# Kernel optimization log

Measured on AMD Instinct MI355X. Metric: run time of the kernel, lower is better.

Reference implementation:

```python
import jax, jax.numpy as jnp
import numpy as np

D = 768   # embedding_dimensions (richness) — hardcoded in source
H = 3     # heads — hardcoded in source


def setup_inputs() -> dict:
    key = jax.random.key(0)
    ks = jax.random.split(key, 12)
    s = 1.0 / np.sqrt(D)
    s3 = 1.0 / np.sqrt(H * D)
    return {
        "x": jax.random.normal(ks[0], (4, 2048, D), dtype=jnp.float32),
        # QKV projections: Linear(D, D*H), stored as (in, out)
        "Wq": jax.random.uniform(ks[1], (D, D * H), jnp.float32, -s, s),
        "bq": jax.random.uniform(ks[2], (D * H,), jnp.float32, -s, s),
        "Wk": jax.random.uniform(ks[3], (D, D * H), jnp.float32, -s, s),
        "bk": jax.random.uniform(ks[4], (D * H,), jnp.float32, -s, s),
        "Wv": jax.random.uniform(ks[5], (D, D * H), jnp.float32, -s, s),
        "bv": jax.random.uniform(ks[6], (D * H,), jnp.float32, -s, s),
        # final projection: Linear(H*D, D)
        "Wo": jax.random.uniform(ks[7], (H * D, D), jnp.float32, -s3, s3),
        "bo": jax.random.uniform(ks[8], (D,), jnp.float32, -s3, s3),
        # FFN: Linear(D, D) + LeakyReLU
        "Wf": jax.random.uniform(ks[9], (D, D), jnp.float32, -s, s),
        "bf": jax.random.uniform(ks[10], (D,), jnp.float32, -s, s),
    }


def reference(x, Wq, bq, Wk, bk, Wv, bv, Wo, bo, Wf, bf):
    B, S, _ = x.shape
    # QKV: [B,S,H*D] -> [B,H,S,D]  (head dim == full D, as in source)
    q = (x @ Wq + bq).reshape(B, S, H, D).transpose(0, 2, 1, 3)
    k = (x @ Wk + bk).reshape(B, S, H, D).transpose(0, 2, 1, 3)
    v = (x @ Wv + bv).reshape(B, S, H, D).transpose(0, 2, 1, 3)
    # unscaled attention scores (source applies no 1/sqrt(d))
    scores = jnp.einsum('bhqd,bhkd->bhqk', q, k)
    # faithful masking: tril of the scores themselves, fill zeros with -99999
    masked = jnp.where(jnp.tril(scores) == 0, jnp.float32(-99999.0), scores)
    attn = jax.nn.softmax(masked, axis=-1)
    o = jnp.einsum('bhqk,bhkd->bhqd', attn, v)
    o = o.transpose(0, 2, 1, 3).reshape(B, S, H * D)
    a = o @ Wo + bo
    # "normalisation": subtract global mean over the whole tensor
    n = a - jnp.mean(a)
    y = n + x  # residual
    return jax.nn.leaky_relu(y @ Wf + bf, negative_slope=0.01)
```

## Files before the change

kernel.cpp:

```cpp
#include <hip/hip_runtime.h>
#include <hip/hip_bf16.h>

typedef __attribute__((ext_vector_type(8))) __bf16 bf16x8;
typedef __attribute__((ext_vector_type(4))) float f32x4;
typedef unsigned short u16;

#define DEV static __device__ __forceinline__

#define BAR() asm volatile("s_barrier" ::: "memory")
#define LGKM0() asm volatile("s_waitcnt lgkmcnt(0)" ::: "memory")
#define VMCNT6() asm volatile("s_waitcnt vmcnt(6)" ::: "memory")
#define VMCNT3() asm volatile("s_waitcnt vmcnt(3)" ::: "memory")
#define VMCNT0() asm volatile("s_waitcnt vmcnt(0)" ::: "memory")

DEV void load_lds16(const void* g, void* l) {
  __builtin_amdgcn_global_load_lds(
      (const __attribute__((address_space(1))) unsigned int*)g,
      (__attribute__((address_space(3))) unsigned int*)l, 16, 0, 0);
}

DEV u16 bf16bits(float v) {
  __hip_bfloat16 h = __float2bfloat16(v);
  return __builtin_bit_cast(u16, h);
}

DEV float bf2f(u16 u) {
  return __builtin_bit_cast(float, (unsigned)u << 16);
}

DEV bf16x8 rdfrag(const u16* region, int row, int ks, int l) {
  const int cb = (((ks << 6) | ((l >> 4) << 4)) ^ ((l & 7) << 4));
  return *(const bf16x8*)((const char*)region + row * 128 + cb);
}

struct OffN { unsigned long long a[12], b[12], c[12]; };

enum { G128_SC = 0, G128_PV = 1, G128_PLAIN = 2, G128_LEAKY = 3 };

__global__ __launch_bounds__(512, 1) void k_qkv256(
    const u16* __restrict__ A, const u16* __restrict__ B,
    const float* __restrict__ bias, u16* __restrict__ C, u16* __restrict__ Vt)
{
  int flat = blockIdx.y * 27 + blockIdx.x;
  flat = (flat & 7) * 108 + (flat >> 3);
  const int n0 = (flat % 27) * 256, m0 = (flat / 27) * 256;
  const int lda = 768, ldb = 768, nkt = 12;

  __shared__ u16 smem[65536];
  u16* As0 = smem;
  u16* Bs0 = smem + 32768;

  const int tid = threadIdx.x;
  const int l = tid & 63;
  const int wid = tid >> 6;
  const int wm = wid >> 1, wn = wid & 1;

  const int r0s = wid * 16 + (l >> 3);
  const int ces = ((l & 7) ^ (l >> 3)) << 3;
  const size_t aR0 = (size_t)(m0 + r0s) * lda + ces;
  const size_t aR1 = aR0 + (size_t)8 * lda;
  const size_t bR0 = (size_t)(n0 + r0s) * ldb + ces;
  const size_t bR1 = bR0 + (size_t)8 * ldb;
  const size_t hA = (size_t)128 * lda, hB = (size_t)128 * ldb;
  const int dst0 = wid * 1024 + l * 8, dst1 = dst0 + 512;

#define STAGE_A(bf, h, kkv) do {                                 \
    u16* Lp = As0 + (bf) * 16384 + (h) * 8192;                   \
    load_lds16(A + aR0 + ((h) ? hA : 0) + (kkv), Lp + dst0);     \
    load_lds16(A + aR1 + ((h) ? hA : 0) + (kkv), Lp + dst1);     \
  } while (0)
#define STAGE_B(bf, h, kkv) do {                                 \
    u16* Lp = Bs0 + (bf) * 16384 + (h) * 8192;                   \
    load_lds16(B + bR0 + ((h) ? hB : 0) + (kkv), Lp + dst0);     \
    load_lds16(B + bR1 + ((h) ? hB : 0) + (kkv), Lp + dst1);     \
  } while (0)

  f32x4 acc[2][2][2][4] = {};
  bf16x8 af[2][2], bA[4][2], bB[4][2];

#define MFMA16(QM, QN, BARR)                                                  \
    __builtin_amdgcn_s_setprio(1);                                            \
    _Pragma("unroll") for (int ks = 0; ks < 2; ks++)                          \
      _Pragma("unroll") for (int fm = 0; fm < 2; fm++)                        \
        _Pragma("unroll") for (int fn = 0; fn < 4; fn++)                      \
          acc[QM][QN][fm][fn] = __builtin_amdgcn_mfma_f32_16x16x32_bf16(      \
              af[fm][ks], BARR[fn][ks], acc[QM][QN][fm][fn], 0, 0, 0);        \
    __builtin_amdgcn_s_setprio(0);

#define RD_A(half)                                                            \
    _Pragma("unroll") for (int fm = 0; fm < 2; fm++)                          \
      _Pragma("unroll") for (int ks = 0; ks < 2; ks++)                        \
        af[fm][ks] = rdfrag(half, wm * 32 + fm * 16 + (l & 15), ks, l);
#define RD_B(dstv, half)                                                      \
    _Pragma("unroll") for (int fn = 0; fn < 4; fn++)                          \
      _Pragma("unroll") for (int ks = 0; ks < 2; ks++)                        \
        dstv[fn][ks] = rdfrag(half, wn * 64 + fn * 16 + (l & 15), ks, l);

  STAGE_A(0, 0, 0); STAGE_B(0, 0, 0); STAGE_B(0, 1, 0); STAGE_A(0, 1, 0);
  STAGE_A(1, 0, 64); STAGE_B(1, 0, 64); STAGE_B(1, 1, 64);
  VMCNT3();
  BAR();

  for (int t = 0; t < nkt; ++t) {
    const int cur = t & 1, nxt = cur ^ 1;
    const int kk1 = (t + 1) << 6, kk2 = (t + 2) << 6;
    const bool s1 = (t + 1 < nkt), s2 = (t + 2 < nkt);
    RD_A(As0 + cur * 16384);
    RD_B(bA, Bs0 + cur * 16384);
    if (s1) STAGE_A(nxt, 1, kk1);
    BAR(); LGKM0();
    MFMA16(0, 0, bA);
    BAR();
    RD_B(bB, Bs0 + cur * 16384 + 8192);
    if (s2) STAGE_A(cur, 0, kk2);
    BAR(); LGKM0();
    MFMA16(0, 1, bB);
    BAR();
    RD_A(As0 + cur * 16384 + 8192);
    if (s2) STAGE_B(cur, 0, kk2);
    BAR(); LGKM0();
    MFMA16(1, 1, bB);
    BAR();
    if (s2) STAGE_B(cur, 1, kk2);
    BAR();
    MFMA16(1, 0, bA);
    if (s2) { VMCNT3(); } else { VMCNT0(); }
    BAR();
  }
#undef RD_A
#undef RD_B
#undef MFMA16
#undef STAGE_A
#undef STAGE_B

  __syncthreads();
  const int sel = n0 >= 4608 ? 2 : (n0 >= 2304 ? 1 : 0);
  const int r0c = (l >> 4) << 2;
  if (sel == 2) {
#pragma unroll
    for (int Qm = 0; Qm < 2; Qm++)
#pragma unroll
      for (int Qn = 0; Qn < 2; Qn++)
#pragma unroll
        for (int fn = 0; fn < 4; fn++) {
          const int coll = Qn * 128 + wn * 64 + fn * 16 + (l & 15);
          const float bv = bias[n0 + coll];
#pragma unroll
          for (int fm = 0; fm < 2; fm++)
#pragma unroll
            for (int r = 0; r < 4; r++) {
              const int rowl = Qm * 128 + wm * 32 + fm * 16 + r0c + r;
              smem[coll * 256 + (rowl ^ (((coll >> 2) & 3) << 4))] =
                  bf16bits(acc[Qm][Qn][fm][fn][r] + bv);
            }
        }
    __syncthreads();
    const int n0v = n0 - 4608;
    const int h = n0v / 768, d0l = n0v % 768;
    const int b = m0 >> 11, sbase = m0 & 2047;
    u16* Cb = Vt + ((size_t)(b * 3 + h) * 768 + d0l) * 2048 + sbase;
#pragma unroll
    for (int j = 0; j < 16; j++) {
      const int dr = j * 16 + (tid >> 5);
      const int c = (tid & 31) * 8;
      bf16x8 v = *(const bf16x8*)&smem[dr * 256 + (c ^ (((dr >> 2) & 3) << 4))];
      *(bf16x8*)&Cb[(size_t)dr * 2048 + c] = v;
    }
  } else {
#pragma unroll
    for (int Qm = 0; Qm < 2; Qm++)
#pragma unroll
      for (int Qn = 0; Qn < 2; Qn++)
#pragma unroll
        for (int fn = 0; fn < 4; fn++) {
          const int coll = Qn * 128 + wn * 64 + fn * 16 + (l & 15);
          const float bv = bias[n0 + coll];
#pragma unroll
          for (int fm = 0; fm < 2; fm++)
#pragma unroll
            for (int r = 0; r < 4; r++) {
              const int rowl = Qm * 128 + wm * 32 + fm * 16 + r0c + r;
              smem[rowl * 256 + (coll ^ (((rowl >> 2) & 3) << 4))] =
                  bf16bits(acc[Qm][Qn][fm][fn][r] + bv);
            }
        }
    __syncthreads();
    u16* Cb = C + (size_t)sel * (8192ull * 2304) + (n0 - sel * 2304);
#pragma unroll
    for (int j = 0; j < 16; j++) {
      const int rowl = j * 16 + (tid >> 5);
      const int c = (tid & 31) * 8;
      bf16x8 v = *(const bf16x8*)&smem[rowl * 256 + (c ^ (((rowl >> 2) & 3) << 4))];
      *(bf16x8*)&Cb[(size_t)(m0 + rowl) * 2304 + c] = v;
    }
  }
}

template<int MODE>
__global__ __launch_bounds__(512, 1) void k_g128(
    const u16* __restrict__ Abase, const u16* __restrict__ Bbase,
    const float* __restrict__ bias, void* __restrict__ Cbase,
    float* __restrict__ part,
    long lda, long ldb, long ldc, int K, OffN off)
{
  int m0, n0, z, r = 0, rb = 0, nkt, arow0, brow0;
  const u16 *A, *B;
  if (MODE == G128_SC) {
    r = blockIdx.y; z = blockIdx.z;
    rb = r >> 1;
    if ((int)blockIdx.x > rb) return;
    m0 = r * 128; n0 = blockIdx.x * 256;
    nkt = K >> 6;
    A = Abase + off.a[z]; B = Bbase + off.b[z];
    arow0 = m0; brow0 = n0;
  } else if (MODE == G128_PV) {
    r = 15 - (int)blockIdx.y;
    rb = r >> 1;
    z = blockIdx.x / 3;
    m0 = r * 128; n0 = (blockIdx.x % 3) * 256;
    nkt = (rb + 1) * 4;
    lda = (long)(rb + 1) * 256;
    A = Abase + off.a[z] + (size_t)32768 * rb * (rb + 1);
    B = Bbase + off.b[z];
    arow0 = (r & 1) * 128; brow0 = n0;
  } else {
    z = 0;
    m0 = blockIdx.y * 128; n0 = blockIdx.x * 256;
    nkt = K >> 6;
    A = Abase; B = Bbase;
    arow0 = m0; brow0 = n0;
  }

  __shared__ u16 smem[73728];

  const int tid = threadIdx.x;
  const int l = tid & 63;
  const int wid = tid >> 6;
  const int wm = wid & 1;
  const int wn = wid >> 1;

  const int ces = ((tid & 7) ^ ((tid >> 3) & 7)) << 3;
  const u16* aS = A + (size_t)(arow0 + (tid >> 3)) * lda + ces;
  const u16* bS = B + (size_t)(brow0 + (tid >> 3)) * ldb + ces;
  const int t8 = tid * 8;

#define STG(buf, kkv) do {                                       \
    u16* Lp = smem + (buf) * 24576;                              \
    load_lds16(aS + (kkv),             Lp + t8);                 \
    load_lds16(aS + 64 * lda + (kkv),  Lp + 4096 + t8);          \
    load_lds16(bS + (kkv),             Lp + 8192 + t8);          \
    load_lds16(bS + 64 * ldb + (kkv),  Lp + 12288 + t8);         \
    load_lds16(bS + 128 * ldb + (kkv), Lp + 16384 + t8);         \
    load_lds16(bS + 192 * ldb + (kkv), Lp + 20480 + t8);         \
  } while (0)

  f32x4 acc[4][4] = {};
  bf16x8 af[4][2], bf[4][2];

  STG(0, 0);
  STG(1, 64);
  VMCNT6();
  BAR();

  for (int t = 0; t < nkt; ++t) {
    const u16* Ar = smem + (t % 3) * 24576;
    const u16* Br = Ar + 8192;
#pragma unroll
    for (int fm = 0; fm < 4; fm++)
#pragma unroll
      for (int ks = 0; ks < 2; ks++)
        af[fm][ks] = rdfrag(Ar, wm * 64 + fm * 16 + (l & 15), ks, l);
#pragma unroll
    for (int fn = 0; fn < 4; fn++)
#pragma unroll
      for (int ks = 0; ks < 2; ks++)
        bf[fn][ks] = rdfrag(Br, wn * 64 + fn * 16 + (l & 15), ks, l);
    const bool s2 = (t + 2 < nkt);
    if (s2) STG((t + 2) % 3, (t + 2) << 6);
    BAR(); LGKM0();
    __builtin_amdgcn_s_setprio(1);
#pragma unroll
    for (int ks = 0; ks < 2; ks++)
#pragma unroll
      for (int fm = 0; fm < 4; fm++)
#pragma unroll
        for (int fn = 0; fn < 4; fn++)
          acc[fm][fn] = __builtin_amdgcn_mfma_f32_16x16x32_bf16(
              af[fm][ks], bf[fn][ks], acc[fm][fn], 0, 0, 0);
    __builtin_amdgcn_s_setprio(0);
    if (s2) { VMCNT6(); } else if (t + 1 < nkt) { VMCNT0(); }
    BAR();
  }
#undef STG

  const int r0c = (l >> 4) << 2;
  if (MODE == G128_SC) {
    float mx4[4][4], s4[4][4];
#pragma unroll
    for (int fm = 0; fm < 4; fm++)
#pragma unroll
      for (int rr = 0; rr < 4; rr++) {
        const int gi = m0 + wm * 64 + fm * 16 + r0c + rr;
        float mv = -1e30f;
#pragma unroll
        for (int fn = 0; fn < 4; fn++) {
          const int gc = n0 + wn * 64 + fn * 16 + (l & 15);
          float v = (gc <= gi) ? acc[fm][fn][rr] : -1e30f;
          acc[fm][fn][rr] = v;
          mv = fmaxf(mv, v);
        }
        mx4[fm][rr] = mv;
      }
#pragma unroll
    for (int o = 1; o < 16; o <<= 1)
#pragma unroll
      for (int fm = 0; fm < 4; fm++)
#pragma unroll
        for (int rr = 0; rr < 4; rr++)
          mx4[fm][rr] = fmaxf(mx4[fm][rr], __shfl_xor(mx4[fm][rr], o, 64));
    float* redm = (float*)smem;
    float* reds = redm + 512;
#pragma unroll
    for (int fm = 0; fm < 4; fm++)
#pragma unroll
      for (int rr = 0; rr < 4; rr++)
        if ((l & 15) == fm * 4 + rr)
          redm[(wm * 64 + fm * 16 + r0c + rr) * 4 + wn] = mx4[fm][rr];
    __syncthreads();
#pragma unroll
    for (int fm = 0; fm < 4; fm++)
#pragma unroll
      for (int rr = 0; rr < 4; rr++) {
        const int rowl = wm * 64 + fm * 16 + r0c + rr;
        f32x4 rm = *(const f32x4*)&redm[rowl * 4];
        const float tm = fmaxf(fmaxf(rm[0], rm[1]), fmaxf(rm[2], rm[3]));
        mx4[fm][rr] = tm;
        float ss = 0.f;
#pragma unroll
        for (int fn = 0; fn < 4; fn++) {
          const float e = expf(acc[fm][fn][rr] - tm);
          acc[fm][fn][rr] = e;
          ss += e;
        }
        s4[fm][rr] = ss;
      }
#pragma unroll
    for (int o = 1; o < 16; o <<= 1)
#pragma unroll
      for (int fm = 0; fm < 4; fm++)
#pragma unroll
        for (int rr = 0; rr < 4; rr++)
          s4[fm][rr] += __shfl_xor(s4[fm][rr], o, 64);
#pragma unroll
    for (int fm = 0; fm < 4; fm++)
#pragma unroll
      for (int rr = 0; rr < 4; rr++)
        if ((l & 15) == fm * 4 + rr)
          reds[(wm * 64 + fm * 16 + r0c + rr) * 4 + wn] = s4[fm][rr];
    __syncthreads();
    if (wn == 0) {
#pragma unroll
      for (int fm = 0; fm < 4; fm++)
#pragma unroll
        for (int rr = 0; rr < 4; rr++)
          if ((l & 15) == fm * 4 + rr) {
            const int rowl = wm * 64 + fm * 16 + r0c + rr;
            f32x4 rs = *(const f32x4*)&reds[rowl * 4];
            float2 pw;
            pw.x = mx4[fm][rr];
            pw.y = rs[0] + rs[1] + rs[2] + rs[3];
            *(float2*)&part[(size_t)z * 32768 +
                            ((size_t)(m0 + rowl) * 8 + blockIdx.x) * 2] = pw;
          }
    }
    __syncthreads();
#pragma unroll
    for (int fn = 0; fn < 4; fn++) {
      const int coll = wn * 64 + fn * 16 + (l & 15);
#pragma unroll
      for (int fm = 0; fm < 4; fm++)
#pragma unroll
        for (int rr = 0; rr < 4; rr++) {
          const int rowl = wm * 64 + fm * 16 + r0c + rr;
          smem[rowl * 256 + (coll ^ (((rowl >> 2) & 3) << 4))] =
              bf16bits(acc[fm][fn][rr]);
        }
    }
    __syncthreads();
    u16* Cb = (u16*)Cbase + off.c[z] + (size_t)32768 * rb * (rb + 1);
    const int W = (rb + 1) << 8;
    const int pr0 = (r & 1) * 128;
#pragma unroll
    for (int j = 0; j < 8; j++) {
      const int rowl = j * 16 + (tid >> 5);
      const int c = (tid & 31) * 8;
      bf16x8 v = *(const bf16x8*)&smem[rowl * 256 + (c ^ (((rowl >> 2) & 3) << 4))];
      *(bf16x8*)&Cb[(size_t)(pr0 + rowl) * W + n0 + c] = v;
    }
  } else if (MODE == G128_PV) {
    __syncthreads();
#pragma unroll
    for (int fn = 0; fn < 4; fn++) {
      const int coll = wn * 64 + fn * 16 + (l & 15);
#pragma unroll
      for (int fm = 0; fm < 4; fm++)
#pragma unroll
        for (int rr = 0; rr < 4; rr++) {
          const int rowl = wm * 64 + fm * 16 + r0c + rr;
          smem[rowl * 256 + (coll ^ (((rowl >> 2) & 3) << 4))] =
              bf16bits(acc[fm][fn][rr]);
        }
    }
    __syncthreads();
    u16* Cb = (u16*)Cbase + off.c[z] + n0;
#pragma unroll
    for (int j = 0; j < 8; j++) {
      const int rowl = j * 16 + (tid >> 5);
      const int c = (tid & 31) * 8;
      bf16x8 v = *(const bf16x8*)&smem[rowl * 256 + (c ^ (((rowl >> 2) & 3) << 4))];
      *(bf16x8*)&Cb[(size_t)(m0 + rowl) * 2304 + c] = v;
    }
  } else {
#pragma unroll
    for (int fn = 0; fn < 4; fn++) {
      const int col = n0 + wn * 64 + fn * 16 + (l & 15);
      const float bv = bias[col];
#pragma unroll
      for (int fm = 0; fm < 4; fm++)
#pragma unroll
        for (int rr = 0; rr < 4; rr++) {
          const int rowl = wm * 64 + fm * 16 + r0c + rr;
          float v = acc[fm][fn][rr] + bv;
          if (MODE == G128_LEAKY) v = v > 0.f ? v : 0.01f * v;
          ((float*)Cbase)[(size_t)(m0 + rowl) * ldc + col] = v;
        }
    }
  }
}

__global__ __launch_bounds__(256) void k_cast_x(const float* __restrict__ in,
                                                u16* __restrict__ out) {
  const size_t i = ((size_t)blockIdx.x * 256 + threadIdx.x) * 4;
  float4 v = *(const float4*)&in[i];
  ushort4 o;
  o.x = bf16bits(v.x); o.y = bf16bits(v.y); o.z = bf16bits(v.z); o.w = bf16bits(v.w);
  *(ushort4*)&out[i] = o;
}

__global__ __launch_bounds__(256) void k_wt(const float* __restrict__ in,
                                            u16* __restrict__ out, int R, int C) {
  __shared__ float tile[32][33];
  const int c0 = blockIdx.x * 32, r0 = blockIdx.y * 32;
  const int tx = threadIdx.x, ty = threadIdx.y;
#pragma unroll
  for (int k = 0; k < 4; k++)
    tile[ty + 8 * k][tx] = in[(size_t)(r0 + ty + 8 * k) * C + c0 + tx];
  __syncthreads();
#pragma unroll
  for (int k = 0; k < 4; k++)
    out[(size_t)(c0 + ty + 8 * k) * R + r0 + tx] = bf16bits(tile[tx][ty + 8 * k]);
}

__global__ __launch_bounds__(256) void k_bias_concat(const float* __restrict__ bq,
                                                     const float* __restrict__ bk,
                                                     const float* __restrict__ bv,
                                                     float* __restrict__ out) {
  const int i = blockIdx.x * 256 + threadIdx.x;
  if (i < 2304) out[i] = bq[i];
  else if (i < 4608) out[i] = bk[i - 2304];
  else if (i < 6912) out[i] = bv[i - 4608];
}

__global__ __launch_bounds__(256) void k_rescale(u16* __restrict__ P,
                                                 const float* __restrict__ part) {
  const int w = threadIdx.x >> 6, l = threadIdx.x & 63;
  const int gi = blockIdx.x * 4 + w;
  const int z = blockIdx.y;
  const int rb = gi >> 8;
  const int W = (rb + 1) << 8;
  const float2* pp = (const float2*)part + (size_t)z * 16384 + (size_t)gi * 8;
  float m = -1e30f;
#pragma unroll
  for (int t = 0; t < 8; t++)
    if (t <= rb) m = fmaxf(m, pp[t].x);
  float den = 0.f;
#pragma unroll
  for (int t = 0; t < 8; t++)
    if (t <= rb) den += pp[t].y * expf(pp[t].x - m);
  const float inv = 1.f / den;
  u16* Prow = P + (size_t)z * 2359296 + (size_t)32768 * rb * (rb + 1) +
              (size_t)(gi & 255) * W;
#pragma unroll
  for (int t = 0; t < 8; t++)
    if (t <= rb) {
      const float ft = expf(pp[t].x - m) * inv;
      ushort4 v = *(const ushort4*)&Prow[t * 256 + l * 4];
      v.x = bf16bits(bf2f(v.x) * ft);
      v.y = bf16bits(bf2f(v.y) * ft);
      v.z = bf16bits(bf2f(v.z) * ft);
      v.w = bf16bits(bf2f(v.w) * ft);
      *(ushort4*)&Prow[t * 256 + l * 4] = v;
    }
}

__global__ __launch_bounds__(256) void k_red1(const float* __restrict__ a,
                                              float* __restrict__ part) {
  float s = 0.f;
  for (size_t idx = (size_t)blockIdx.x * 256 + threadIdx.x; idx < 6291456ull; idx += 2048ull * 256)
    s += a[idx];
#pragma unroll
  for (int o = 32; o >= 1; o >>= 1) s += __shfl_xor(s, o, 64);
  __shared__ float r[4];
  const int t = threadIdx.x, w = t >> 6;
  if ((t & 63) == 0) r[w] = s;
  __syncthreads();
  if (t == 0) part[blockIdx.x] = r[0] + r[1] + r[2] + r[3];
}

__global__ __launch_bounds__(256) void k_red2(const float* __restrict__ part,
                                              float* __restrict__ mean) {
  const int t = threadIdx.x;
  float s = 0.f;
  for (int i = t; i < 2048; i += 256) s += part[i];
#pragma unroll
  for (int o = 32; o >= 1; o >>= 1) s += __shfl_xor(s, o, 64);
  __shared__ float r[4];
  const int w = t >> 6;
  if ((t & 63) == 0) r[w] = s;
  __syncthreads();
  if (t == 0) mean[0] = (r[0] + r[1] + r[2] + r[3]) * (1.f / 6291456.f);
}

__global__ __launch_bounds__(256) void k_residual(const float* __restrict__ a,
                                                  const float* __restrict__ x,
                                                  const float* __restrict__ meanp,
                                                  u16* __restrict__ yb) {
  const float mean = meanp[0];
  const size_t i = ((size_t)blockIdx.x * 256 + threadIdx.x) * 4;
  float4 av = *(const float4*)&a[i];
  float4 xv = *(const float4*)&x[i];
  ushort4 o;
  o.x = bf16bits(av.x - mean + xv.x);
  o.y = bf16bits(av.y - mean + xv.y);
  o.z = bf16bits(av.z - mean + xv.z);
  o.w = bf16bits(av.w - mean + xv.w);
  *(ushort4*)&yb[i] = o;
}

extern "C" void kernel_launch(void* const* d_in, const int* in_sizes, int n_in,
                              void* d_out, int out_size, void* d_ws, size_t ws_size,
                              hipStream_t stream) {
  const float* x   = (const float*)d_in[0];
  const float* Wq  = (const float*)d_in[1];
  const float* bq  = (const float*)d_in[2];
  const float* Wk  = (const float*)d_in[3];
  const float* bk  = (const float*)d_in[4];
  const float* Wv  = (const float*)d_in[5];
  const float* bv  = (const float*)d_in[6];
  const float* Wo  = (const float*)d_in[7];
  const float* bo  = (const float*)d_in[8];
  const float* Wf  = (const float*)d_in[9];
  const float* bfb = (const float*)d_in[10];

  char* ws = (char*)d_ws;
  const size_t MSZ    = 37748736;
  const size_t o_Wqkvt = 0;
  const size_t o_Wot  = 10616832;
  const size_t o_Wft  = o_Wot + 3538944;
  const size_t o_bqkv = o_Wft + 1179648;
  const size_t o_prt  = o_bqkv + 32768;
  const size_t o_mn   = o_prt + 8192;
  const size_t o_part = o_mn + 256;
  const size_t o_xb   = o_part + 1572864;
  const size_t o_Q    = o_xb + 12582912;
  const size_t o_K    = o_Q + MSZ;
  const size_t o_Vt   = o_K + MSZ;
  const size_t o_P    = o_Vt + MSZ;
  const size_t o_end  = o_P + 56623104;
  if (ws_size < o_end) return;

  const size_t o_O  = o_Q;
  const size_t o_a  = o_K;
  const size_t o_yb = o_xb;

  OffN z0{};
  dim3 b32(32, 8);

  k_cast_x<<<6144, 256, 0, stream>>>(x, (u16*)(ws + o_xb));
  k_wt<<<dim3(72, 24), b32, 0, stream>>>(Wq, (u16*)(ws + o_Wqkvt), 768, 2304);
  k_wt<<<dim3(72, 24), b32, 0, stream>>>(Wk, (u16*)(ws + o_Wqkvt) + 2304 * 768, 768, 2304);
  k_wt<<<dim3(72, 24), b32, 0, stream>>>(Wv, (u16*)(ws + o_Wqkvt) + 2 * 2304 * 768, 768, 2304);
  k_wt<<<dim3(24, 72), b32, 0, stream>>>(Wo, (u16*)(ws + o_Wot), 2304, 768);
  k_wt<<<dim3(24, 24), b32, 0, stream>>>(Wf, (u16*)(ws + o_Wft), 768, 768);
  k_bias_concat<<<27, 256, 0, stream>>>(bq, bk, bv, (float*)(ws + o_bqkv));

  k_qkv256<<<dim3(27, 32), 512, 0, stream>>>(
      (const u16*)(ws + o_xb), (const u16*)(ws + o_Wqkvt),
      (const float*)(ws + o_bqkv), (u16*)(ws + o_Q), (u16*)(ws + o_Vt));

  OffN so{}, po{};
  for (int zz = 0; zz < 12; zz++) {
    const int b = zz / 3, h = zz % 3;
    so.a[zz] = (size_t)b * 2048 * 2304 + (size_t)h * 768;
    so.b[zz] = so.a[zz];
    so.c[zz] = (size_t)zz * 2359296;
    po.a[zz] = so.c[zz];
    po.b[zz] = (size_t)zz * 768 * 2048;
    po.c[zz] = so.a[zz];
  }
  k_g128<G128_SC><<<dim3(8, 16, 12), 512, 0, stream>>>(
      (const u16*)(ws + o_Q), (const u16*)(ws + o_K), nullptr, ws + o_P,
      (float*)(ws + o_part), 2304, 2304, 0, 768, so);
  k_rescale<<<dim3(512, 12), 256, 0, stream>>>((u16*)(ws + o_P),
                                               (const float*)(ws + o_part));
  k_g128<G128_PV><<<dim3(36, 16), 512, 0, stream>>>(
      (const u16*)(ws + o_P), (const u16*)(ws + o_Vt), nullptr, ws + o_O,
      nullptr, 0, 2048, 0, 0, po);

  k_g128<G128_PLAIN><<<dim3(3, 64), 512, 0, stream>>>(
      (const u16*)(ws + o_O), (const u16*)(ws + o_Wot), bo, ws + o_a,
      nullptr, 2304, 2304, 768, 2304, z0);

  k_red1<<<2048, 256, 0, stream>>>((const float*)(ws + o_a), (float*)(ws + o_prt));
  k_red2<<<1, 256, 0, stream>>>((const float*)(ws + o_prt), (float*)(ws + o_mn));
  k_residual<<<6144, 256, 0, stream>>>((const float*)(ws + o_a), x,
                                       (const float*)(ws + o_mn), (u16*)(ws + o_yb));

  k_g128<G128_LEAKY><<<dim3(3, 64), 512, 0, stream>>>(
      (const u16*)(ws + o_yb), (const u16*)(ws + o_Wft), bfb, d_out,
      nullptr, 768, 768, 768, 768, z0);
}
```

Before: 436.7 us.

## Halve k_g128 K-tile to 32 to cut LDS and raise occupancy, use fast exp

The generic 128x256 GEMM kernel now stages 32-wide K slices instead of 64, with a new swizzle and fragment reader. This halves the triple-buffered LDS footprint, and launch bounds now permit up to four blocks per CU instead of one. The price is twice as many barriers and pipeline iterations per tile. The softmax and rescale kernels switch expf to __expf, and the V-transpose epilogue in the QKV kernel gets a different LDS swizzle to reduce bank conflicts.

Result: faster. 418.3 us (-4.2%).

```diff
diff --git a/kernel.cpp b/kernel.cpp
--- a/kernel.cpp
+++ b/kernel.cpp
@@ -9,7 +9,6 @@
 
 #define BAR() asm volatile("s_barrier" ::: "memory")
 #define LGKM0() asm volatile("s_waitcnt lgkmcnt(0)" ::: "memory")
-#define VMCNT6() asm volatile("s_waitcnt vmcnt(6)" ::: "memory")
 #define VMCNT3() asm volatile("s_waitcnt vmcnt(3)" ::: "memory")
 #define VMCNT0() asm volatile("s_waitcnt vmcnt(0)" ::: "memory")
 
@@ -31,6 +30,11 @@
 DEV bf16x8 rdfrag(const u16* region, int row, int ks, int l) {
   const int cb = (((ks << 6) | ((l >> 4) << 4)) ^ ((l & 7) << 4));
   return *(const bf16x8*)((const char*)region + row * 128 + cb);
+}
+
+DEV bf16x8 rdfrag32(const u16* region, int row, int l) {
+  const int cb = (((l >> 4) ^ (row & 3)) << 4);
+  return *(const bf16x8*)((const char*)region + row * 64 + cb);
 }
 
 struct OffN { unsigned long long a[12], b[12], c[12]; };
@@ -150,7 +154,7 @@
 #pragma unroll
             for (int r = 0; r < 4; r++) {
               const int rowl = Qm * 128 + wm * 32 + fm * 16 + r0c + r;
-              smem[coll * 256 + (rowl ^ (((coll >> 2) & 3) << 4))] =
+              smem[coll * 256 + ((((rowl >> 3) ^ (coll & 7)) << 3) | (rowl & 7))] =
                   bf16bits(acc[Qm][Qn][fm][fn][r] + bv);
             }
         }
@@ -162,9 +166,9 @@
 #pragma unroll
     for (int j = 0; j < 16; j++) {
       const int dr = j * 16 + (tid >> 5);
-      const int c = (tid & 31) * 8;
-      bf16x8 v = *(const bf16x8*)&smem[dr * 256 + (c ^ (((dr >> 2) & 3) << 4))];
-      *(bf16x8*)&Cb[(size_t)dr * 2048 + c] = v;
+      const int c8 = tid & 31;
+      bf16x8 v = *(const bf16x8*)&smem[dr * 256 + ((c8 ^ (dr & 7)) << 3)];
+      *(bf16x8*)&Cb[(size_t)dr * 2048 + c8 * 8] = v;
     }
   } else {
 #pragma unroll
@@ -197,7 +201,7 @@
 }
 
 template<int MODE>
-__global__ __launch_bounds__(512, 1) void k_g128(
+__global__ __launch_bounds__(512, 4) void k_g128(
     const u16* __restrict__ Abase, const u16* __restrict__ Bbase,
     const float* __restrict__ bias, void* __restrict__ Cbase,
     float* __restrict__ part,
@@ -210,7 +214,7 @@
     rb = r >> 1;
     if ((int)blockIdx.x > rb) return;
     m0 = r * 128; n0 = blockIdx.x * 256;
-    nkt = K >> 6;
+    nkt = K >> 5;
     A = Abase + off.a[z]; B = Bbase + off.b[z];
     arow0 = m0; brow0 = n0;
   } else if (MODE == G128_PV) {
@@ -218,7 +222,7 @@
     rb = r >> 1;
     z = blockIdx.x / 3;
     m0 = r * 128; n0 = (blockIdx.x % 3) * 256;
-    nkt = (rb + 1) * 4;
+    nkt = (rb + 1) * 8;
     lda = (long)(rb + 1) * 256;
     A = Abase + off.a[z] + (size_t)32768 * rb * (rb + 1);
     B = Bbase + off.b[z];
@@ -226,12 +230,12 @@
   } else {
     z = 0;
     m0 = blockIdx.y * 128; n0 = blockIdx.x * 256;
-    nkt = K >> 6;
+    nkt = K >> 5;
     A = Abase; B = Bbase;
     arow0 = m0; brow0 = n0;
   }
 
-  __shared__ u16 smem[73728];
+  __shared__ u16 smem[36864];
 
   const int tid = threadIdx.x;
   const int l = tid & 63;
@@ -239,56 +243,48 @@
   const int wm = wid & 1;
   const int wn = wid >> 1;
 
-  const int ces = ((tid & 7) ^ ((tid >> 3) & 7)) << 3;
-  const u16* aS = A + (size_t)(arow0 + (tid >> 3)) * lda + ces;
-  const u16* bS = B + (size_t)(brow0 + (tid >> 3)) * ldb + ces;
+  const int ces = (((tid & 3) ^ ((tid >> 2) & 3)) << 3);
+  const u16* aS  = A + (size_t)(arow0 + (tid >> 2)) * lda + ces;
+  const u16* bS0 = B + (size_t)(brow0 + (tid >> 2)) * ldb + ces;
+  const u16* bS1 = bS0 + (size_t)128 * ldb;
   const int t8 = tid * 8;
 
-#define STG(buf, kkv) do {                                       \
-    u16* Lp = smem + (buf) * 24576;                              \
-    load_lds16(aS + (kkv),             Lp + t8);                 \
-    load_lds16(aS + 64 * lda + (kkv),  Lp + 4096 + t8);          \
-    load_lds16(bS + (kkv),             Lp + 8192 + t8);          \
-    load_lds16(bS + 64 * ldb + (kkv),  Lp + 12288 + t8);         \
-    load_lds16(bS + 128 * ldb + (kkv), Lp + 16384 + t8);         \
-    load_lds16(bS + 192 * ldb + (kkv), Lp + 20480 + t8);         \
+#define STG(buf, kkv) do {                         \
+    u16* Lp = smem + (buf) * 12288;                \
+    load_lds16(aS  + (kkv), Lp + t8);              \
+    load_lds16(bS0 + (kkv), Lp + 4096 + t8);       \
+    load_lds16(bS1 + (kkv), Lp + 8192 + t8);       \
   } while (0)
 
   f32x4 acc[4][4] = {};
-  bf16x8 af[4][2], bf[4][2];
+  bf16x8 af[4], bf[4];
 
   STG(0, 0);
-  STG(1, 64);
-  VMCNT6();
+  STG(1, 32);
+  VMCNT3();
   BAR();
 
   for (int t = 0; t < nkt; ++t) {
-    const u16* Ar = smem + (t % 3) * 24576;
-    const u16* Br = Ar + 8192;
+    const u16* Ar = smem + (t % 3) * 12288;
+    const u16* Br = Ar + 4096;
 #pragma unroll
     for (int fm = 0; fm < 4; fm++)
-#pragma unroll
-      for (int ks = 0; ks < 2; ks++)
-        af[fm][ks] = rdfrag(Ar, wm * 64 + fm * 16 + (l & 15), ks, l);
+      af[fm] = rdfrag32(Ar, wm * 64 + fm * 16 + (l & 15), l);
 #pragma unroll
     for (int fn = 0; fn < 4; fn++)
-#pragma unroll
-      for (int ks = 0; ks < 2; ks++)
-        bf[fn][ks] = rdfrag(Br, wn * 64 + fn * 16 + (l & 15), ks, l);
+      bf[fn] = rdfrag32(Br, wn * 64 + fn * 16 + (l & 15), l);
     const bool s2 = (t + 2 < nkt);
-    if (s2) STG((t + 2) % 3, (t + 2) << 6);
+    if (s2) STG((t + 2) % 3, (t + 2) << 5);
     BAR(); LGKM0();
     __builtin_amdgcn_s_setprio(1);
 #pragma unroll
-    for (int ks = 0; ks < 2; ks++)
-#pragma unroll
-      for (int fm = 0; fm < 4; fm++)
-#pragma unroll
-        for (int fn = 0; fn < 4; fn++)
-          acc[fm][fn] = __builtin_amdgcn_mfma_f32_16x16x32_bf16(
-              af[fm][ks], bf[fn][ks], acc[fm][fn], 0, 0, 0);
+    for (int fm = 0; fm < 4; fm++)
+#pragma unroll
+      for (int fn = 0; fn < 4; fn++)
+        acc[fm][fn] = __builtin_amdgcn_mfma_f32_16x16x32_bf16(
+            af[fm], bf[fn], acc[fm][fn], 0, 0, 0);
     __builtin_amdgcn_s_setprio(0);
-    if (s2) { VMCNT6(); } else if (t + 1 < nkt) { VMCNT0(); }
+    if (s2) { VMCNT3(); } else if (t + 1 < nkt) { VMCNT0(); }
     BAR();
   }
 #undef STG
@@ -338,7 +334,7 @@
         float ss = 0.f;
 #pragma unroll
         for (int fn = 0; fn < 4; fn++) {
-          const float e = expf(acc[fm][fn][rr] - tm);
+          const float e = __expf(acc[fm][fn][rr] - tm);
           acc[fm][fn][rr] = e;
           ss += e;
         }
@@ -486,14 +482,14 @@
   float den = 0.f;
 #pragma unroll
   for (int t = 0; t < 8; t++)
-    if (t <= rb) den += pp[t].y * expf(pp[t].x - m);
+    if (t <= rb) den += pp[t].y * __expf(pp[t].x - m);
   const float inv = 1.f / den;
   u16* Prow = P + (size_t)z * 2359296 + (size_t)32768 * rb * (rb + 1) +
               (size_t)(gi & 255) * W;
 #pragma unroll
   for (int t = 0; t < 8; t++)
     if (t <= rb) {
-      const float ft = expf(pp[t].x - m) * inv;
+      const float ft = __expf(pp[t].x - m) * inv;
       ushort4 v = *(const ushort4*)&Prow[t * 256 + l * 4];
       v.x = bf16bits(bf2f(v.x) * ft);
       v.y = bf16bits(bf2f(v.y) * ft);
```
